# Optimization experiments

Hardware: AMD Instinct MI355X
Metric: run time of the kernel (lower is better)

The kernel has to match this reference:

```python
import jax, jax.numpy as jnp
import numpy as np

B, S, V, H, O = 2048, 512, 32128, 16, 16


def setup_inputs() -> dict:
    key = jax.random.key(0)
    ks = jax.random.split(key, 7)
    x = jax.random.randint(ks[0], (B, S), 0, V)  # token ids
    enc1_w = jax.random.normal(ks[1], (H, V), dtype=jnp.float32) * 0.02
    enc1_b = jax.random.normal(ks[2], (H,), dtype=jnp.float32) * 0.02
    mean_w = jax.random.normal(ks[3], (O, H), dtype=jnp.float32) * 0.1
    mean_b = jax.random.normal(ks[4], (O,), dtype=jnp.float32) * 0.1
    logvar_w = jax.random.normal(ks[5], (O, H), dtype=jnp.float32) * 0.1
    logvar_b = jax.random.normal(ks[6], (O,), dtype=jnp.float32) * 0.1
    return {"x": x, "enc1_w": enc1_w, "enc1_b": enc1_b,
            "mean_w": mean_w, "mean_b": mean_b,
            "logvar_w": logvar_w, "logvar_b": logvar_b}


def reference(x, enc1_w, enc1_b, mean_w, mean_b, logvar_w, logvar_b):
    # one_hot(x, V).float().sum(1) == per-row token-count histogram [B, V]
    # (avoids materializing the [B, S, V] one-hot tensor)
    b, s = x.shape
    counts = jnp.zeros((b, V), dtype=jnp.float32).at[
        jnp.arange(b)[:, None], x].add(1.0)
    h = jax.nn.relu(counts @ enc1_w.T + enc1_b)  # [B, H]
    mean = h @ mean_w.T + mean_b                 # [B, O]
    logvar = h @ logvar_w.T + logvar_b           # [B, O]
    return (mean, logvar)
```

## Files before the change

kernel.cpp:

```cpp
#include <hip/hip_runtime.h>

#define B_ 2048
#define S_ 512
#define V_ 32128
#define H_ 16
#define O_ 16

__device__ __forceinline__ unsigned bf16rne(float f) {
    unsigned x = __float_as_uint(f);
    return (x + 0x7fffu + ((x >> 16) & 1u)) >> 16;
}

__global__ __launch_bounds__(256) void transpose_w_bf16_kernel(
    const float* __restrict__ w,
    uint4* __restrict__ wT)
{
    const int col = blockIdx.x * 256 + threadIdx.x;
    if (col >= V_) return;

    float r[16];
#pragma unroll
    for (int h = 0; h < 16; ++h) r[h] = w[(size_t)h * V_ + col];

    unsigned u[8];
#pragma unroll
    for (int k = 0; k < 8; ++k)
        u[k] = bf16rne(r[2 * k]) | (bf16rne(r[2 * k + 1]) << 16);

    wT[(size_t)col * 2 + 0] = make_uint4(u[0], u[1], u[2], u[3]);
    wT[(size_t)col * 2 + 1] = make_uint4(u[4], u[5], u[6], u[7]);
}

__global__ __launch_bounds__(256) void encoder_bf16_kernel(
    const int*   __restrict__ x,
    const uint4* __restrict__ wT,
    const float* __restrict__ enc1_b,
    const float* __restrict__ mean_w,
    const float* __restrict__ mean_b,
    const float* __restrict__ logvar_w,
    const float* __restrict__ logvar_b,
    float*       __restrict__ out)
{
    const int t    = threadIdx.x;
    const int wave = t >> 6;
    const int lane = t & 63;
    const int b    = blockIdx.x * 4 + wave;

    const int g = lane >> 1;
    const int p = lane & 1;

    const int    o   = lane & 15;
    const int    sel = (lane >> 4) & 1;
    const float* Wrow = (sel ? logvar_w : mean_w) + o * 16;
    float4 w0 = ((const float4*)Wrow)[0];
    float4 w1 = ((const float4*)Wrow)[1];
    float4 w2 = ((const float4*)Wrow)[2];
    float4 w3 = ((const float4*)Wrow)[3];
    float  bv = (sel ? logvar_b : mean_b)[o];
    float4 eb = ((const float4*)enc1_b)[p * 2 + 0];
    float4 eb2 = ((const float4*)enc1_b)[p * 2 + 1];

    const int* xr = x + (size_t)b * S_;
    int v[16];
#pragma unroll
    for (int j = 0; j < 16; ++j)
        v[j] = __builtin_nontemporal_load(xr + j * 32 + g);

    float a[8];
#pragma unroll
    for (int k = 0; k < 8; ++k) a[k] = 0.0f;
#pragma unroll
    for (int j = 0; j < 16; ++j) {
        uint4 wv = wT[(size_t)v[j] * 2 + p];
        a[0] += __uint_as_float(wv.x << 16);
        a[1] += __uint_as_float(wv.x & 0xffff0000u);
        a[2] += __uint_as_float(wv.y << 16);
        a[3] += __uint_as_float(wv.y & 0xffff0000u);
        a[4] += __uint_as_float(wv.z << 16);
        a[5] += __uint_as_float(wv.z & 0xffff0000u);
        a[6] += __uint_as_float(wv.w << 16);
        a[7] += __uint_as_float(wv.w & 0xffff0000u);
    }

#pragma unroll
    for (int m = 2; m <= 32; m <<= 1) {
#pragma unroll
        for (int k = 0; k < 8; ++k) a[k] += __shfl_xor(a[k], m);
    }

    const float ebv[8] = {eb.x, eb.y, eb.z, eb.w, eb2.x, eb2.y, eb2.z, eb2.w};
    float hs[8];
#pragma unroll
    for (int k = 0; k < 8; ++k) hs[k] = fmaxf(a[k] + ebv[k], 0.0f);

    float ho[8];
#pragma unroll
    for (int k = 0; k < 8; ++k) ho[k] = __shfl_xor(hs[k], 1);

    float hv[16];
#pragma unroll
    for (int k = 0; k < 8; ++k) {
        hv[k]     = p ? ho[k] : hs[k];
        hv[8 + k] = p ? hs[k] : ho[k];
    }

    if (lane < 32) {
        float s = bv;
        s += w0.x * hv[0]  + w0.y * hv[1]  + w0.z * hv[2]  + w0.w * hv[3];
        s += w1.x * hv[4]  + w1.y * hv[5]  + w1.z * hv[6]  + w1.w * hv[7];
        s += w2.x * hv[8]  + w2.y * hv[9]  + w2.z * hv[10] + w2.w * hv[11];
        s += w3.x * hv[12] + w3.y * hv[13] + w3.z * hv[14] + w3.w * hv[15];
        __builtin_nontemporal_store(
            s, out + (size_t)sel * B_ * O_ + (size_t)b * O_ + o);
    }
}

__global__ __launch_bounds__(256) void encoder_f32_fallback_kernel(
    const int*   __restrict__ x,
    const float* __restrict__ table,
    const float* __restrict__ enc1_b,
    const float* __restrict__ mean_w,
    const float* __restrict__ mean_b,
    const float* __restrict__ logvar_w,
    const float* __restrict__ logvar_b,
    float*       __restrict__ out)
{
    __shared__ int   toks[S_];
    __shared__ float hred[4][16];
    __shared__ float hvec[16];

    const int t = threadIdx.x;
    const int b = blockIdx.x;
    {
        const int2* xr = (const int2*)(x + (size_t)b * S_);
        ((int2*)toks)[t] = xr[t];
    }
    __syncthreads();

    const int q = t & 3;
    const int g = t >> 2;
    float a0 = 0.f, a1 = 0.f, a2 = 0.f, a3 = 0.f;
#pragma unroll
    for (int j = 0; j < 8; ++j) {
        int v = toks[j * 64 + g];
        a0 += table[(size_t)(q * 4 + 0) * V_ + v];
        a1 += table[(size_t)(q * 4 + 1) * V_ + v];
        a2 += table[(size_t)(q * 4 + 2) * V_ + v];
        a3 += table[(size_t)(q * 4 + 3) * V_ + v];
    }
#pragma unroll
    for (int m = 4; m <= 32; m <<= 1) {
        a0 += __shfl_xor(a0, m);
        a1 += __shfl_xor(a1, m);
        a2 += __shfl_xor(a2, m);
        a3 += __shfl_xor(a3, m);
    }
    const int wave = t >> 6;
    const int lane = t & 63;
    if (lane < 4) {
        hred[wave][lane * 4 + 0] = a0;
        hred[wave][lane * 4 + 1] = a1;
        hred[wave][lane * 4 + 2] = a2;
        hred[wave][lane * 4 + 3] = a3;
    }
    __syncthreads();
    if (t < 16) {
        float s = hred[0][t] + hred[1][t] + hred[2][t] + hred[3][t] + enc1_b[t];
        hvec[t] = fmaxf(s, 0.0f);
    }
    __syncthreads();
    if (t < 32) {
        const int    o  = t & 15;
        const float* W  = (t < 16) ? mean_w : logvar_w;
        const float* Bv = (t < 16) ? mean_b : logvar_b;
        float s = Bv[o];
#pragma unroll
        for (int k = 0; k < 16; ++k) s += W[o * 16 + k] * hvec[k];
        const size_t off = (t < 16) ? 0 : (size_t)B_ * O_;
        out[off + (size_t)b * O_ + o] = s;
    }
}

extern "C" void kernel_launch(void* const* d_in, const int* in_sizes, int n_in,
                              void* d_out, int out_size, void* d_ws, size_t ws_size,
                              hipStream_t stream) {
    const int*   x        = (const int*)d_in[0];
    const float* enc1_w   = (const float*)d_in[1];
    const float* enc1_b   = (const float*)d_in[2];
    const float* mean_w   = (const float*)d_in[3];
    const float* mean_b   = (const float*)d_in[4];
    const float* logvar_w = (const float*)d_in[5];
    const float* logvar_b = (const float*)d_in[6];
    float*       out      = (float*)d_out;

    const size_t wT_bytes = (size_t)V_ * H_ * 2;
    if (ws_size >= wT_bytes) {
        uint4* wT = (uint4*)d_ws;
        transpose_w_bf16_kernel<<<(V_ + 255) / 256, 256, 0, stream>>>(enc1_w, wT);
        encoder_bf16_kernel<<<B_ / 4, 256, 0, stream>>>(
            x, wT, enc1_b, mean_w, mean_b, logvar_w, logvar_b, out);
    } else {
        encoder_f32_fallback_kernel<<<B_, 256, 0, stream>>>(
            x, enc1_w, enc1_b, mean_w, mean_b, logvar_w, logvar_b, out);
    }
}
```

Measured before the change: 16.94 us.

## Split each row across two waves and shrink transpose blocks to 64 threads

The encoder kernel now gives each batch row two waves, each gathering half of the 512 tokens, and combines the two partial hidden vectors through shared memory after a block barrier. This doubles the number of waves and blocks to expose more memory-level parallelism for the latency-bound gather. The bias handling and ReLU move to after the cross-wave sum. The transpose kernel switches to 64-thread blocks with no bounds check, relying on V being divisible by 64, which spreads it over more CUs. The cost is an extra LDS round-trip and a __syncthreads per block.

```diff
diff --git a/kernel.cpp b/kernel.cpp
--- a/kernel.cpp
+++ b/kernel.cpp
@@ -11,12 +11,11 @@
     return (x + 0x7fffu + ((x >> 16) & 1u)) >> 16;
 }
 
-__global__ __launch_bounds__(256) void transpose_w_bf16_kernel(
+__global__ __launch_bounds__(64) void transpose_w_bf16_kernel(
     const float* __restrict__ w,
     uint4* __restrict__ wT)
 {
-    const int col = blockIdx.x * 256 + threadIdx.x;
-    if (col >= V_) return;
+    const int col = blockIdx.x * 64 + threadIdx.x;
 
     float r[16];
 #pragma unroll
@@ -41,10 +40,14 @@
     const float* __restrict__ logvar_b,
     float*       __restrict__ out)
 {
+    __shared__ float hred[4][16];
+
     const int t    = threadIdx.x;
     const int wave = t >> 6;
     const int lane = t & 63;
-    const int b    = blockIdx.x * 4 + wave;
+    const int rib  = wave >> 1;
+    const int half = wave & 1;
+    const int b    = blockIdx.x * 2 + rib;
 
     const int g = lane >> 1;
     const int p = lane & 1;
@@ -56,21 +59,23 @@
     float4 w1 = ((const float4*)Wrow)[1];
     float4 w2 = ((const float4*)Wrow)[2];
     float4 w3 = ((const float4*)Wrow)[3];
-    float  bv = (sel ? logvar_b : mean_b)[o];
-    float4 eb = ((const float4*)enc1_b)[p * 2 + 0];
-    float4 eb2 = ((const float4*)enc1_b)[p * 2 + 1];
-
-    const int* xr = x + (size_t)b * S_;
-    int v[16];
-#pragma unroll
-    for (int j = 0; j < 16; ++j)
+    float  bv  = (sel ? logvar_b : mean_b)[o];
+    float4 eb0 = ((const float4*)enc1_b)[0];
+    float4 eb1 = ((const float4*)enc1_b)[1];
+    float4 eb2 = ((const float4*)enc1_b)[2];
+    float4 eb3 = ((const float4*)enc1_b)[3];
+
+    const int* xr = x + (size_t)b * S_ + half * 256;
+    int v[8];
+#pragma unroll
+    for (int j = 0; j < 8; ++j)
         v[j] = __builtin_nontemporal_load(xr + j * 32 + g);
 
     float a[8];
 #pragma unroll
     for (int k = 0; k < 8; ++k) a[k] = 0.0f;
 #pragma unroll
-    for (int j = 0; j < 16; ++j) {
+    for (int j = 0; j < 8; ++j) {
         uint4 wv = wT[(size_t)v[j] * 2 + p];
         a[0] += __uint_as_float(wv.x << 16);
         a[1] += __uint_as_float(wv.x & 0xffff0000u);
@@ -88,23 +93,23 @@
         for (int k = 0; k < 8; ++k) a[k] += __shfl_xor(a[k], m);
     }
 
-    const float ebv[8] = {eb.x, eb.y, eb.z, eb.w, eb2.x, eb2.y, eb2.z, eb2.w};
-    float hs[8];
-#pragma unroll
-    for (int k = 0; k < 8; ++k) hs[k] = fmaxf(a[k] + ebv[k], 0.0f);
-
-    float ho[8];
-#pragma unroll
-    for (int k = 0; k < 8; ++k) ho[k] = __shfl_xor(hs[k], 1);
-
-    float hv[16];
-#pragma unroll
-    for (int k = 0; k < 8; ++k) {
-        hv[k]     = p ? ho[k] : hs[k];
-        hv[8 + k] = p ? hs[k] : ho[k];
-    }
-
-    if (lane < 32) {
+    if (lane < 2) {
+#pragma unroll
+        for (int k = 0; k < 8; ++k) hred[wave][p * 8 + k] = a[k];
+    }
+    __syncthreads();
+
+    if (half == 0 && lane < 32) {
+        const float ebv[16] = {eb0.x, eb0.y, eb0.z, eb0.w,
+                               eb1.x, eb1.y, eb1.z, eb1.w,
+                               eb2.x, eb2.y, eb2.z, eb2.w,
+                               eb3.x, eb3.y, eb3.z, eb3.w};
+        float hv[16];
+#pragma unroll
+        for (int i = 0; i < 16; ++i) {
+            float s = hred[wave][i] + hred[wave + 1][i] + ebv[i];
+            hv[i] = fmaxf(s, 0.0f);
+        }
         float s = bv;
         s += w0.x * hv[0]  + w0.y * hv[1]  + w0.z * hv[2]  + w0.w * hv[3];
         s += w1.x * hv[4]  + w1.y * hv[5]  + w1.z * hv[6]  + w1.w * hv[7];
@@ -196,8 +201,8 @@
     const size_t wT_bytes = (size_t)V_ * H_ * 2;
     if (ws_size >= wT_bytes) {
         uint4* wT = (uint4*)d_ws;
-        transpose_w_bf16_kernel<<<(V_ + 255) / 256, 256, 0, stream>>>(enc1_w, wT);
-        encoder_bf16_kernel<<<B_ / 4, 256, 0, stream>>>(
+        transpose_w_bf16_kernel<<<V_ / 64, 64, 0, stream>>>(enc1_w, wT);
+        encoder_bf16_kernel<<<B_ / 2, 256, 0, stream>>>(
             x, wT, enc1_b, mean_w, mean_b, logvar_w, logvar_b, out);
     } else {
         encoder_f32_fallback_kernel<<<B_, 256, 0, stream>>>(
```

Result: no change. 17.26 us (+1.9%).

## Fuse weight transpose and encoder into one launch with inter-block flag sync

Applied to the files above, without the earlier changes.

Merges the bf16 weight-transpose kernel and the encoder kernel into a single launch. The first 126 blocks convert weights and publish per-block magic flags with release stores. The encoder blocks load their tokens, then spin on those flags with acquire loads before gathering rows. This removes a separate kernel launch and the gap between the two launches. In exchange, transpose writes become per-dword atomic stores, and progress depends on producer blocks being scheduled alongside waiting blocks. The flags are never reset, so on repeated calls consumers may not wait for the current transpose and can read the previous call's table.

```diff
diff --git a/kernel.cpp b/kernel.cpp
--- a/kernel.cpp
+++ b/kernel.cpp
@@ -6,45 +6,55 @@
 #define H_ 16
 #define O_ 16
 
+#define TB_ 126
+#define EB_ (B_ / 4)
+#define MAGIC_(i) (0x5EED0C0Du ^ (unsigned)(i))
+
 __device__ __forceinline__ unsigned bf16rne(float f) {
     unsigned x = __float_as_uint(f);
     return (x + 0x7fffu + ((x >> 16) & 1u)) >> 16;
 }
 
-__global__ __launch_bounds__(256) void transpose_w_bf16_kernel(
+__global__ __launch_bounds__(256) void fused_encoder_kernel(
+    const int*   __restrict__ x,
     const float* __restrict__ w,
-    uint4* __restrict__ wT)
-{
-    const int col = blockIdx.x * 256 + threadIdx.x;
-    if (col >= V_) return;
-
-    float r[16];
-#pragma unroll
-    for (int h = 0; h < 16; ++h) r[h] = w[(size_t)h * V_ + col];
-
-    unsigned u[8];
-#pragma unroll
-    for (int k = 0; k < 8; ++k)
-        u[k] = bf16rne(r[2 * k]) | (bf16rne(r[2 * k + 1]) << 16);
-
-    wT[(size_t)col * 2 + 0] = make_uint4(u[0], u[1], u[2], u[3]);
-    wT[(size_t)col * 2 + 1] = make_uint4(u[4], u[5], u[6], u[7]);
-}
-
-__global__ __launch_bounds__(256) void encoder_bf16_kernel(
-    const int*   __restrict__ x,
-    const uint4* __restrict__ wT,
     const float* __restrict__ enc1_b,
     const float* __restrict__ mean_w,
     const float* __restrict__ mean_b,
     const float* __restrict__ logvar_w,
     const float* __restrict__ logvar_b,
+    unsigned*    __restrict__ wT,
+    unsigned*    __restrict__ marks,
     float*       __restrict__ out)
 {
-    const int t    = threadIdx.x;
+    const int t   = threadIdx.x;
+    const int blk = blockIdx.x;
+
+    if (blk < TB_) {
+        const int col = blk * 256 + t;
+        if (col < V_) {
+            float r[16];
+#pragma unroll
+            for (int h = 0; h < 16; ++h) r[h] = w[(size_t)h * V_ + col];
+            unsigned* dst = wT + (size_t)col * 8;
+#pragma unroll
+            for (int k = 0; k < 8; ++k) {
+                unsigned u = bf16rne(r[2 * k]) | (bf16rne(r[2 * k + 1]) << 16);
+                __hip_atomic_store(dst + k, u, __ATOMIC_RELAXED,
+                                   __HIP_MEMORY_SCOPE_AGENT);
+            }
+        }
+        __syncthreads();
+        if (t == 0)
+            __hip_atomic_store(&marks[blk], MAGIC_(blk), __ATOMIC_RELEASE,
+                               __HIP_MEMORY_SCOPE_AGENT);
+        return;
+    }
+
+    const int eb   = blk - TB_;
     const int wave = t >> 6;
     const int lane = t & 63;
-    const int b    = blockIdx.x * 4 + wave;
+    const int b    = eb * 4 + wave;
 
     const int g = lane >> 1;
     const int p = lane & 1;
@@ -57,8 +67,8 @@
     float4 w2 = ((const float4*)Wrow)[2];
     float4 w3 = ((const float4*)Wrow)[3];
     float  bv = (sel ? logvar_b : mean_b)[o];
-    float4 eb = ((const float4*)enc1_b)[p * 2 + 0];
-    float4 eb2 = ((const float4*)enc1_b)[p * 2 + 1];
+    float4 eb0 = ((const float4*)enc1_b)[p * 2 + 0];
+    float4 eb1 = ((const float4*)enc1_b)[p * 2 + 1];
 
     const int* xr = x + (size_t)b * S_;
     int v[16];
@@ -66,12 +76,30 @@
     for (int j = 0; j < 16; ++j)
         v[j] = __builtin_nontemporal_load(xr + j * 32 + g);
 
+    {
+        bool waited = false;
+        const int s0 = (lane < TB_) ? lane : 0;
+        const int s1 = (lane + 64 < TB_) ? lane + 64 : 0;
+        for (;;) {
+            unsigned m0 = __hip_atomic_load(&marks[s0], __ATOMIC_ACQUIRE,
+                                            __HIP_MEMORY_SCOPE_AGENT);
+            unsigned m1 = __hip_atomic_load(&marks[s1], __ATOMIC_ACQUIRE,
+                                            __HIP_MEMORY_SCOPE_AGENT);
+            bool ok = (m0 == MAGIC_(s0)) && (m1 == MAGIC_(s1));
+            if (__all(ok)) break;
+            waited = true;
+            __builtin_amdgcn_s_sleep(8);
+        }
+        if (waited) __threadfence();
+    }
+
+    const uint4* wT4 = (const uint4*)wT;
     float a[8];
 #pragma unroll
     for (int k = 0; k < 8; ++k) a[k] = 0.0f;
 #pragma unroll
     for (int j = 0; j < 16; ++j) {
-        uint4 wv = wT[(size_t)v[j] * 2 + p];
+        uint4 wv = wT4[(size_t)v[j] * 2 + p];
         a[0] += __uint_as_float(wv.x << 16);
         a[1] += __uint_as_float(wv.x & 0xffff0000u);
         a[2] += __uint_as_float(wv.y << 16);
@@ -88,7 +116,8 @@
         for (int k = 0; k < 8; ++k) a[k] += __shfl_xor(a[k], m);
     }
 
-    const float ebv[8] = {eb.x, eb.y, eb.z, eb.w, eb2.x, eb2.y, eb2.z, eb2.w};
+    const float ebv[8] = {eb0.x, eb0.y, eb0.z, eb0.w,
+                          eb1.x, eb1.y, eb1.z, eb1.w};
     float hs[8];
 #pragma unroll
     for (int k = 0; k < 8; ++k) hs[k] = fmaxf(a[k] + ebv[k], 0.0f);
@@ -193,12 +222,14 @@
     const float* logvar_b = (const float*)d_in[6];
     float*       out      = (float*)d_out;
 
-    const size_t wT_bytes = (size_t)V_ * H_ * 2;
-    if (ws_size >= wT_bytes) {
-        uint4* wT = (uint4*)d_ws;
-        transpose_w_bf16_kernel<<<(V_ + 255) / 256, 256, 0, stream>>>(enc1_w, wT);
-        encoder_bf16_kernel<<<B_ / 4, 256, 0, stream>>>(
-            x, wT, enc1_b, mean_w, mean_b, logvar_w, logvar_b, out);
+    const size_t wT_bytes   = (size_t)V_ * H_ * 2;
+    const size_t need_bytes = wT_bytes + TB_ * sizeof(unsigned);
+    if (ws_size >= need_bytes) {
+        unsigned* wT    = (unsigned*)d_ws;
+        unsigned* marks = (unsigned*)((char*)d_ws + wT_bytes);
+        fused_encoder_kernel<<<TB_ + EB_, 256, 0, stream>>>(
+            x, enc1_w, enc1_b, mean_w, mean_b, logvar_w, logvar_b,
+            wT, marks, out);
     } else {
         encoder_f32_fallback_kernel<<<B_, 256, 0, stream>>>(
             x, enc1_w, enc1_b, mean_w, mean_b, logvar_w, logvar_b, out);
```

After: 47.27 us. +179.0%, slower.
